# Kernel tuning notes

Measured on AMD Instinct MI355X. Metric: run time of the kernel, lower is better.

## Reference

```python
import jax, jax.numpy as jnp
import numpy as np

N, D, E, K, CAP = 16384, 1024, 64, 2, 640

def setup_inputs() -> dict:
    key = jax.random.key(0)
    k1, k2, k3 = jax.random.split(key, 3)
    x = jax.random.normal(k1, (N, D), dtype=jnp.float32)
    Wr = jax.random.normal(k2, (D, E), dtype=jnp.float32) / np.sqrt(D)
    br = jnp.zeros((E,), dtype=jnp.float32)
    We = jax.random.normal(k3, (E, D, D), dtype=jnp.float32) / np.sqrt(D)
    return {"x": x, "Wr": Wr, "br": br, "We": We, "k": K, "capacity": CAP}

def _route(x, Wr, br, k, num_experts):
    logits = x @ Wr + br                                  # [N, E]
    top_k_vals, top_k_idxs = jax.lax.top_k(logits, k)     # [N, k]
    gates = jax.nn.softmax(top_k_vals, axis=-1)           # [N, k]
    # flatten k-major like the original: transpose((1,0)).flatten()
    flat = top_k_idxs.T.reshape(-1)                       # [k*N]
    expert_mask = (flat[:, None] == jnp.arange(num_experts)).astype(jnp.int32)
    buffer_idxs = jnp.cumsum(expert_mask, axis=0) * expert_mask - 1  # [k*N, E]
    buffer_idxs = buffer_idxs.reshape(k, -1, num_experts)            # [k, N, E]
    dispatch_idxs = buffer_idxs.transpose(2, 0, 1).max(axis=1)       # [E, N]
    combine_idxs = buffer_idxs.max(axis=-1).T                        # [N, k]
    return gates, top_k_idxs, dispatch_idxs, combine_idxs

def reference(x, Wr, br, We, k, capacity):
    num_experts = Wr.shape[1]
    gates, top_k_idxs, dispatch_idxs, combine_idxs = _route(x, Wr, br, k, num_experts)
    # dispatch: scatter tokens into per-expert capacity buffers; unassigned (-1)
    # and overflow (>= capacity) tokens land in the dropped slot `capacity`.
    d_idx = jnp.where((dispatch_idxs < 0) | (dispatch_idxs > capacity), capacity, dispatch_idxs)
    def scatter_one(idx):
        return jnp.zeros((capacity + 1, x.shape[-1]), x.dtype).at[idx].set(x)[:-1]
    dispatched = jax.vmap(scatter_one)(d_idx)             # [E, C, D]
    # per-expert linear (the wrap()/vmap-ed expert), grouped GEMM
    expert_out = jax.nn.relu(jnp.einsum('ecd,edh->ech', dispatched, We))
    # combine: gather back, pad row `capacity` yields zeros for dropped tokens
    padded = jnp.pad(expert_out, ((0, 0), (0, 1), (0, 0)))
    c_idx = jnp.where((combine_idxs < 0) | (combine_idxs > capacity), capacity, combine_idxs)
    combined = padded[top_k_idxs, c_idx]                  # [N, k, D]
    return jnp.einsum('nk,nkd->nd', gates, combined)      # [N, D]
```

## Files before the change

kernel.cpp:

```cpp
#include <hip/hip_runtime.h>
#include <hip/hip_bf16.h>
#include <cstdint>
#include <cstddef>

#define N_TOK 16384
#define DIM   1024
#define NEXP  64
#define CAPACITY 640

typedef __bf16 bf16x8 __attribute__((ext_vector_type(8)));
typedef float  f32x4  __attribute__((ext_vector_type(4)));

__device__ __forceinline__ unsigned short f2bf(float f) {
    union { float f; unsigned int u; } a; a.f = f;
    unsigned int r = a.u + 0x7FFFu + ((a.u >> 16) & 1u);
    return (unsigned short)(r >> 16);
}

__global__ __launch_bounds__(256) void router_kernel(
    const float* __restrict__ x, const float* __restrict__ Wr,
    const float* __restrict__ br, unsigned short* __restrict__ xb,
    int* __restrict__ top2i, float* __restrict__ gates2)
{
    __shared__ float xs[64][68];
    __shared__ float wT[64][68];
    const int tid = threadIdx.x;
    const int t0  = blockIdx.x * 64;
    const int tm  = tid >> 4;
    const int te  = tid & 15;

    float acc[4][4];
#pragma unroll
    for (int i = 0; i < 4; i++)
#pragma unroll
        for (int j = 0; j < 4; j++) acc[i][j] = 0.f;

    for (int ks = 0; ks < DIM; ks += 64) {
        __syncthreads();
#pragma unroll
        for (int l = 0; l < 4; l++) {
            int row = l * 16 + tm;
            int col = te * 4;
            float4 v = *(const float4*)(x + (size_t)(t0 + row) * DIM + ks + col);
            *(float4*)&xs[row][col] = v;
            ushort4 b = make_ushort4(f2bf(v.x), f2bf(v.y), f2bf(v.z), f2bf(v.w));
            *(ushort4*)(xb + (size_t)(t0 + row) * DIM + ks + col) = b;
        }
#pragma unroll
        for (int l = 0; l < 4; l++) {
            int kr = l * 16 + tm;
            int ec = te * 4;
            float4 v = *(const float4*)(Wr + (size_t)(ks + kr) * NEXP + ec);
            wT[ec + 0][kr] = v.x; wT[ec + 1][kr] = v.y;
            wT[ec + 2][kr] = v.z; wT[ec + 3][kr] = v.w;
        }
        __syncthreads();
#pragma unroll 4
        for (int kk = 0; kk < 64; kk += 4) {
            float4 xv[4], wv[4];
#pragma unroll
            for (int i = 0; i < 4; i++) xv[i] = *(float4*)&xs[tm + i * 16][kk];
#pragma unroll
            for (int j = 0; j < 4; j++) wv[j] = *(float4*)&wT[te + j * 16][kk];
#pragma unroll
            for (int i = 0; i < 4; i++)
#pragma unroll
                for (int j = 0; j < 4; j++)
                    acc[i][j] += xv[i].x * wv[j].x + xv[i].y * wv[j].y +
                                 xv[i].z * wv[j].z + xv[i].w * wv[j].w;
        }
    }
    __syncthreads();
#pragma unroll
    for (int i = 0; i < 4; i++)
#pragma unroll
        for (int j = 0; j < 4; j++)
            xs[tm + i * 16][te + j * 16] = acc[i][j] + br[te + j * 16];
    __syncthreads();
    if (tid < 64) {
        int n = t0 + tid;
        float v1 = -1e30f, v2 = -1e30f; int i1 = 0, i2 = 0;
        for (int e = 0; e < 64; e++) {
            float v = xs[tid][e];
            if (v > v1)      { v2 = v1; i2 = i1; v1 = v; i1 = e; }
            else if (v > v2) { v2 = v;  i2 = e; }
        }
        float g0 = 1.f / (1.f + expf(v2 - v1));
        top2i[n * 2 + 0] = i1; top2i[n * 2 + 1] = i2;
        gates2[n * 2 + 0] = g0; gates2[n * 2 + 1] = 1.f - g0;
    }
}

__global__ __launch_bounds__(256) void hist_kernel(
    const int* __restrict__ top2i, int* __restrict__ hist)
{
    __shared__ int cnt[NEXP];
    int tid = threadIdx.x;
    if (tid < NEXP) cnt[tid] = 0;
    __syncthreads();
    int p = blockIdx.x * 256 + tid;
    int k = p >> 14, n = p & 16383;
    int e = top2i[n * 2 + k];
    atomicAdd(&cnt[e], 1);
    __syncthreads();
    if (tid < NEXP) hist[blockIdx.x * NEXP + tid] = cnt[tid];
}

__global__ __launch_bounds__(64) void scan_kernel(
    const int* __restrict__ hist, int* __restrict__ pre, int* __restrict__ cntc)
{
    int e = threadIdx.x;
    int run = 0;
#pragma unroll 8
    for (int c = 0; c < 128; c++) {
        pre[c * NEXP + e] = run;
        run += hist[c * NEXP + e];
    }
    cntc[e] = run < CAPACITY ? run : CAPACITY;
}

__global__ __launch_bounds__(64) void rank_kernel(
    const int* __restrict__ top2i, const float* __restrict__ gates2,
    const int* __restrict__ pre, int* __restrict__ list_tok,
    float* __restrict__ list_gate)
{
    int lane = threadIdx.x;
    int c = blockIdx.x;
    int cnt_reg = pre[c * NEXP + lane];
    unsigned long long below = (1ull << lane) - 1ull;
    for (int r = 0; r < 4; r++) {
        int p = c * 256 + r * 64 + lane;
        int k = p >> 14, n = p & 16383;
        int e = top2i[n * 2 + k];
        int slot = 0;
#pragma unroll 1
        for (int q = 0; q < NEXP; q++) {
            unsigned long long mask = __ballot(e == q);
            int base = __shfl(cnt_reg, q);
            if (e == q) slot = base + __popcll(mask & below);
            if (lane == q) cnt_reg += (int)__popcll(mask);
        }
        if (slot < CAPACITY) {
            list_tok[e * CAPACITY + slot]  = n;
            list_gate[e * CAPACITY + slot] = gates2[n * 2 + k];
        }
    }
}

#define MT 128
#define NT 128
#define BK 32
#define LDA 36

__global__ __launch_bounds__(256) void moe_gemm(
    const unsigned short* __restrict__ xb, const float* __restrict__ We,
    const int* __restrict__ list_tok, const float* __restrict__ list_gate,
    const int* __restrict__ cntc, float* __restrict__ out)
{
    const int bid = blockIdx.x;
    const int e   = bid / 40;
    const int rem = bid % 40;
    const int mt  = rem >> 3;
    const int nt  = rem & 7;
    const int cnt = cntc[e];
    if (mt * MT >= cnt) return;
    int valid = cnt - mt * MT; if (valid > MT) valid = MT;

    __shared__ unsigned short As[MT * LDA];
    __shared__ unsigned short Bs[NT * LDA];
    __shared__ int   tok_s[MT];
    __shared__ float gate_s[MT];

    const int tid = threadIdx.x;
    if (tid < MT) {
        int slot = mt * MT + tid;
        bool v = tid < valid;
        tok_s[tid]  = v ? list_tok[e * CAPACITY + slot]  : list_tok[e * CAPACITY];
        gate_s[tid] = v ? list_gate[e * CAPACITY + slot] : 0.f;
    }
    __syncthreads();

    const int arow = tid >> 1, ah = tid & 1;
    const unsigned short* aptr = xb + (size_t)tok_s[arow] * DIM + ah * 16;
    const int bn0 = (tid & 31) * 4;
    const int bkr = (tid >> 5) * 4;
    const float* bptr = We + (size_t)e * DIM * DIM + (size_t)bkr * DIM + nt * NT + bn0;

    f32x4 acc[4][4];
#pragma unroll
    for (int i = 0; i < 4; i++)
#pragma unroll
        for (int j = 0; j < 4; j++) acc[i][j] = (f32x4){0.f, 0.f, 0.f, 0.f};

    const int lane = tid & 63, wave = tid >> 6;
    const int wm = wave >> 1, wn = wave & 1;
    const int fm = lane & 15, kq = lane >> 4;

    for (int ks = 0; ks < DIM; ks += BK) {
        __syncthreads();
        uint4 a0 = *(const uint4*)(aptr + ks);
        uint4 a1 = *(const uint4*)(aptr + ks + 8);
        {
            unsigned short* d = &As[arow * LDA + ah * 16];
            *(uint2*)(d + 0)  = make_uint2(a0.x, a0.y);
            *(uint2*)(d + 4)  = make_uint2(a0.z, a0.w);
            *(uint2*)(d + 8)  = make_uint2(a1.x, a1.y);
            *(uint2*)(d + 12) = make_uint2(a1.z, a1.w);
        }
        {
            float4 b[4];
#pragma unroll
            for (int j = 0; j < 4; j++)
                b[j] = *(const float4*)(bptr + (size_t)(ks + j) * DIM);
            union { float4 v; float f[4]; } u0, u1, u2, u3;
            u0.v = b[0]; u1.v = b[1]; u2.v = b[2]; u3.v = b[3];
#pragma unroll
            for (int cc = 0; cc < 4; cc++) {
                unsigned int lo = (unsigned int)f2bf(u0.f[cc]) | ((unsigned int)f2bf(u1.f[cc]) << 16);
                unsigned int hi = (unsigned int)f2bf(u2.f[cc]) | ((unsigned int)f2bf(u3.f[cc]) << 16);
                *(uint2*)&Bs[(bn0 + cc) * LDA + bkr] = make_uint2(lo, hi);
            }
        }
        __syncthreads();
        union { uint2 u[2]; bf16x8 v; } fa[4], fb[4];
#pragma unroll
        for (int i = 0; i < 4; i++) {
            const unsigned short* s = &As[(wm * 64 + i * 16 + fm) * LDA + kq * 8];
            fa[i].u[0] = *(const uint2*)(s);
            fa[i].u[1] = *(const uint2*)(s + 4);
        }
#pragma unroll
        for (int j = 0; j < 4; j++) {
            const unsigned short* s = &Bs[(wn * 64 + j * 16 + fm) * LDA + kq * 8];
            fb[j].u[0] = *(const uint2*)(s);
            fb[j].u[1] = *(const uint2*)(s + 4);
        }
#pragma unroll
        for (int i = 0; i < 4; i++)
#pragma unroll
            for (int j = 0; j < 4; j++)
                acc[i][j] = __builtin_amdgcn_mfma_f32_16x16x32_bf16(
                    fa[i].v, fb[j].v, acc[i][j], 0, 0, 0);
    }

    const int col0 = nt * NT + wn * 64 + fm;
#pragma unroll
    for (int i = 0; i < 4; i++) {
        int rbase = wm * 64 + i * 16 + kq * 4;
#pragma unroll
        for (int j = 0; j < 4; j++) {
            int col = col0 + j * 16;
#pragma unroll
            for (int r = 0; r < 4; r++) {
                int row = rbase + r;
                if (row < valid) {
                    float v = acc[i][j][r];
                    v = fmaxf(v, 0.f) * gate_s[row];
                    atomicAdd(out + (size_t)tok_s[row] * DIM + col, v);
                }
            }
        }
    }
}

extern "C" void kernel_launch(void* const* d_in, const int* in_sizes, int n_in,
                              void* d_out, int out_size, void* d_ws, size_t ws_size,
                              hipStream_t stream)
{
    const float* x  = (const float*)d_in[0];
    const float* Wr = (const float*)d_in[1];
    const float* br = (const float*)d_in[2];
    const float* We = (const float*)d_in[3];
    float* out = (float*)d_out;

    char* ws = (char*)d_ws;
    size_t off = 0;
    unsigned short* xb = (unsigned short*)(ws + off); off += (size_t)N_TOK * DIM * 2;
    int*   top2i     = (int*)(ws + off);   off += (size_t)N_TOK * 2 * 4;
    float* gates2    = (float*)(ws + off); off += (size_t)N_TOK * 2 * 4;
    int*   hist      = (int*)(ws + off);   off += 128 * NEXP * 4;
    int*   pre       = (int*)(ws + off);   off += 128 * NEXP * 4;
    int*   cntc      = (int*)(ws + off);   off += NEXP * 4;
    int*   list_tok  = (int*)(ws + off);   off += NEXP * CAPACITY * 4;
    float* list_gate = (float*)(ws + off); off += NEXP * CAPACITY * 4;

    hipMemsetAsync(out, 0, (size_t)N_TOK * DIM * 4, stream);
    router_kernel<<<N_TOK / 64, 256, 0, stream>>>(x, Wr, br, xb, top2i, gates2);
    hist_kernel<<<128, 256, 0, stream>>>(top2i, hist);
    scan_kernel<<<1, 64, 0, stream>>>(hist, pre, cntc);
    rank_kernel<<<128, 64, 0, stream>>>(top2i, gates2, pre, list_tok, list_gate);
    moe_gemm<<<NEXP * 40, 256, 0, stream>>>(xb, We, list_tok, list_gate, cntc, out);
}
```

Baseline: 676.9 us.

## Pre-convert expert weights to transposed bf16 and use direct-to-LDS GEMM loads

```diff
diff --git a/kernel.cpp b/kernel.cpp
--- a/kernel.cpp
+++ b/kernel.cpp
@@ -15,6 +15,52 @@
     union { float f; unsigned int u; } a; a.f = f;
     unsigned int r = a.u + 0x7FFFu + ((a.u >> 16) & 1u);
     return (unsigned short)(r >> 16);
+}
+
+typedef __attribute__((address_space(3))) void       lds_void;
+typedef const __attribute__((address_space(1))) void glb_void;
+__device__ __forceinline__ void gload_lds16(const void* g, void* l) {
+    __builtin_amdgcn_global_load_lds((glb_void*)g, (lds_void*)l, 16, 0, 0);
+}
+
+__global__ __launch_bounds__(256) void convert_we(
+    const float* __restrict__ We, unsigned short* __restrict__ Web)
+{
+    __shared__ unsigned int ts[64 * 33];
+    const int bid = blockIdx.x;
+    const int e  = bid >> 8;
+    const int kb = (bid >> 4) & 15, nb = bid & 15;
+    const int k0 = kb * 64, n0 = nb * 64;
+    const int tid = threadIdx.x;
+
+    {
+        const int rp = tid >> 3, ng = tid & 7;
+        const float* r0 = We + (size_t)e * DIM * DIM + (size_t)(k0 + 2 * rp) * DIM + n0 + ng * 8;
+        float4 a0 = *(const float4*)(r0);
+        float4 a1 = *(const float4*)(r0 + 4);
+        float4 b0 = *(const float4*)(r0 + DIM);
+        float4 b1 = *(const float4*)(r0 + DIM + 4);
+        const float* af = (const float*)&a0;
+        const float* bf = (const float*)&b0;
+#pragma unroll
+        for (int i = 0; i < 4; i++)
+            ts[(ng * 8 + i) * 33 + rp] = (unsigned int)f2bf(af[i]) | ((unsigned int)f2bf(bf[i]) << 16);
+        af = (const float*)&a1; bf = (const float*)&b1;
+#pragma unroll
+        for (int i = 0; i < 4; i++)
+            ts[(ng * 8 + 4 + i) * 33 + rp] = (unsigned int)f2bf(af[i]) | ((unsigned int)f2bf(bf[i]) << 16);
+    }
+    __syncthreads();
+    {
+        const int nr = tid >> 2, kg = tid & 3;
+        unsigned int r[8];
+#pragma unroll
+        for (int i = 0; i < 8; i++) r[i] = ts[nr * 33 + kg * 8 + i];
+        unsigned int* dst = (unsigned int*)Web +
+            (((size_t)(e * 1024 + n0 + nr) * DIM + k0) >> 1) + kg * 8;
+        *(uint4*)(dst)     = make_uint4(r[0], r[1], r[2], r[3]);
+        *(uint4*)(dst + 4) = make_uint4(r[4], r[5], r[6], r[7]);
+    }
 }
 
 __global__ __launch_bounds__(256) void router_kernel(
@@ -149,6 +195,112 @@
 
 #define MT 128
 #define NT 128
+#define BKF 64
+
+__global__ __launch_bounds__(256) void moe_gemm_bt(
+    const unsigned short* __restrict__ xb, const unsigned short* __restrict__ Web,
+    const int* __restrict__ list_tok, const float* __restrict__ list_gate,
+    const int* __restrict__ cntc, float* __restrict__ out)
+{
+    const int bid = blockIdx.x;
+    const int e   = bid / 40;
+    const int rem = bid % 40;
+    const int mt  = rem >> 3;
+    const int nt  = rem & 7;
+    const int cnt = cntc[e];
+    if (mt * MT >= cnt) return;
+    int valid = cnt - mt * MT; if (valid > MT) valid = MT;
+
+    __shared__ unsigned short As[MT * BKF];
+    __shared__ unsigned short Bs[NT * BKF];
+    __shared__ int   tok_s[MT];
+    __shared__ float gate_s[MT];
+
+    const int tid = threadIdx.x;
+    if (tid < MT) {
+        int slot = mt * MT + tid;
+        bool v = tid < valid;
+        tok_s[tid]  = v ? list_tok[e * CAPACITY + slot]  : list_tok[e * CAPACITY];
+        gate_s[tid] = v ? list_gate[e * CAPACITY + slot] : 0.f;
+    }
+    __syncthreads();
+
+    const int lane = tid & 63, wave = tid >> 6;
+    const int wm = wave >> 1, wn = wave & 1;
+    const int fm = lane & 15, kq = lane >> 4;
+
+    const int srow = wave * 8 + (lane >> 3);
+    const int q    = (lane & 7) ^ (lane >> 3);
+    const unsigned short* aP[4];
+    const unsigned short* bP[4];
+    unsigned short* aL[4];
+    unsigned short* bL[4];
+#pragma unroll
+    for (int j = 0; j < 4; j++) {
+        int row = j * 32 + srow;
+        aP[j] = xb + (size_t)tok_s[row] * DIM + q * 8;
+        bP[j] = Web + ((size_t)(e * 1024 + nt * NT + row)) * DIM + q * 8;
+        aL[j] = &As[row * BKF + (lane & 7) * 8];
+        bL[j] = &Bs[row * BKF + (lane & 7) * 8];
+    }
+
+    f32x4 acc[4][4];
+#pragma unroll
+    for (int i = 0; i < 4; i++)
+#pragma unroll
+        for (int j = 0; j < 4; j++) acc[i][j] = (f32x4){0.f, 0.f, 0.f, 0.f};
+
+    for (int ks = 0; ks < DIM; ks += BKF) {
+        __syncthreads();
+#pragma unroll
+        for (int j = 0; j < 4; j++) gload_lds16(aP[j] + ks, aL[j]);
+#pragma unroll
+        for (int j = 0; j < 4; j++) gload_lds16(bP[j] + ks, bL[j]);
+        __syncthreads();
+
+#pragma unroll
+        for (int kk = 0; kk < 2; kk++) {
+            const int qq = kk * 4 + kq;
+            union { uint4 u; bf16x8 v; } fa[4], fb[4];
+#pragma unroll
+            for (int i = 0; i < 4; i++) {
+                int r = wm * 64 + i * 16 + fm;
+                fa[i].u = *(const uint4*)&As[r * BKF + (qq ^ (r & 7)) * 8];
+            }
+#pragma unroll
+            for (int j = 0; j < 4; j++) {
+                int r = wn * 64 + j * 16 + fm;
+                fb[j].u = *(const uint4*)&Bs[r * BKF + (qq ^ (r & 7)) * 8];
+            }
+#pragma unroll
+            for (int i = 0; i < 4; i++)
+#pragma unroll
+                for (int j = 0; j < 4; j++)
+                    acc[i][j] = __builtin_amdgcn_mfma_f32_16x16x32_bf16(
+                        fa[i].v, fb[j].v, acc[i][j], 0, 0, 0);
+        }
+    }
+
+    const int col0 = nt * NT + wn * 64 + fm;
+#pragma unroll
+    for (int i = 0; i < 4; i++) {
+        int rbase = wm * 64 + i * 16 + kq * 4;
+#pragma unroll
+        for (int j = 0; j < 4; j++) {
+            int col = col0 + j * 16;
+#pragma unroll
+            for (int r = 0; r < 4; r++) {
+                int row = rbase + r;
+                if (row < valid) {
+                    float v = acc[i][j][r];
+                    v = fmaxf(v, 0.f) * gate_s[row];
+                    atomicAdd(out + (size_t)tok_s[row] * DIM + col, v);
+                }
+            }
+        }
+    }
+}
+
 #define BK 32
 #define LDA 36
 
@@ -283,11 +435,19 @@
     int*   cntc      = (int*)(ws + off);   off += NEXP * 4;
     int*   list_tok  = (int*)(ws + off);   off += NEXP * CAPACITY * 4;
     float* list_gate = (float*)(ws + off); off += NEXP * CAPACITY * 4;
+    off = (off + 255) & ~(size_t)255;
+    unsigned short* Web = (unsigned short*)(ws + off);
+    size_t need = off + (size_t)NEXP * DIM * DIM * 2;
+    const bool fast = ws_size >= need;
 
     hipMemsetAsync(out, 0, (size_t)N_TOK * DIM * 4, stream);
+    if (fast) convert_we<<<NEXP * 256, 256, 0, stream>>>(We, Web);
     router_kernel<<<N_TOK / 64, 256, 0, stream>>>(x, Wr, br, xb, top2i, gates2);
     hist_kernel<<<128, 256, 0, stream>>>(top2i, hist);
     scan_kernel<<<1, 64, 0, stream>>>(hist, pre, cntc);
     rank_kernel<<<128, 64, 0, stream>>>(top2i, gates2, pre, list_tok, list_gate);
-    moe_gemm<<<NEXP * 40, 256, 0, stream>>>(xb, We, list_tok, list_gate, cntc, out);
-}
+    if (fast)
+        moe_gemm_bt<<<NEXP * 40, 256, 0, stream>>>(xb, Web, list_tok, list_gate, cntc, out);
+    else
+        moe_gemm<<<NEXP * 40, 256, 0, stream>>>(xb, We, list_tok, list_gate, cntc, out);
+}
```

Measured after the change: 720.5 us. +6.4%, slower.
